# Performance work log

Measured on AMD Instinct MI355X. Metric: run time of the kernel, lower is better.

The kernel has to match this reference:

```python
import jax, jax.numpy as jnp
import numpy as np

N_NODES = 50000
N_EDGES = 150000
NODE_F, EDGE_F = 4, 11
HID, HID_OUT = 512, 1024
VS, AS_, N_ACT = 2048, 2048, 1000


def _graph_conv(x, W, b, src, dst, n, edge_weight=None):
    # DGL GraphConv, norm='both': D_out^{-1/2} on src feats, sum-aggregate, D_in^{-1/2} on dst.
    deg_out = jnp.maximum(jnp.zeros((n,), x.dtype).at[src].add(1.0), 1.0)
    deg_in = jnp.maximum(jnp.zeros((n,), x.dtype).at[dst].add(1.0), 1.0)
    h = x * (deg_out[:, None] ** -0.5)
    mult_first = W.shape[0] > W.shape[1]
    if mult_first:
        h = h @ W
    m = h[src]  # [E, d] gather
    if edge_weight is not None:
        m = m * edge_weight  # elementwise u_mul_e
    agg = jax.ops.segment_sum(m, dst, num_segments=n)
    if not mult_first:
        agg = agg @ W
    return agg * (deg_in[:, None] ** -0.5) + b


def setup_inputs() -> dict:
    key = jax.random.key(0)
    ks = jax.random.split(key, 16)
    s = 0.05
    return {
        'node_feats': jax.random.normal(ks[0], (N_NODES, NODE_F), jnp.float32),
        'edge_feats': jax.random.normal(ks[1], (N_EDGES, EDGE_F), jnp.float32),
        'W1': jax.random.normal(ks[2], (NODE_F, EDGE_F), jnp.float32) * s,
        'b1': jnp.zeros((EDGE_F,), jnp.float32),
        'W2': jax.random.normal(ks[3], (EDGE_F, HID), jnp.float32) * s,
        'b2': jnp.zeros((HID,), jnp.float32),
        'W3': jax.random.normal(ks[4], (HID, HID_OUT), jnp.float32) * s,
        'b3': jnp.zeros((HID_OUT,), jnp.float32),
        'Wv1': jax.random.normal(ks[5], (HID_OUT, VS), jnp.float32) * s,
        'bv1': jnp.zeros((VS,), jnp.float32),
        'Wv2': jax.random.normal(ks[6], (VS, 1), jnp.float32) * s,
        'bv2': jnp.zeros((1,), jnp.float32),
        'Wa1': jax.random.normal(ks[7], (HID_OUT, AS_), jnp.float32) * s,
        'ba1': jnp.zeros((AS_,), jnp.float32),
        'Wa2': jax.random.normal(ks[8], (AS_, N_ACT), jnp.float32) * s,
        'ba2': jnp.zeros((N_ACT,), jnp.float32),
        'src': jax.random.randint(ks[9], (N_EDGES,), 0, N_NODES, jnp.int32),
        'dst': jax.random.randint(ks[10], (N_EDGES,), 0, N_NODES, jnp.int32),
    }


def reference(node_feats, edge_feats, W1, b1, W2, b2, W3, b3,
              Wv1, bv1, Wv2, bv2, Wa1, ba1, Wa2, ba2, src, dst):
    n = node_feats.shape[0]
    loop = jnp.arange(n, dtype=src.dtype)
    srcL = jnp.concatenate([src, loop])  # add_self_loop
    dstL = jnp.concatenate([dst, loop])
    # self-loop edges get zero edge features (DGL default)
    ef = jnp.concatenate([edge_feats, jnp.zeros((n, edge_feats.shape[1]), edge_feats.dtype)], axis=0)

    h = jax.nn.relu(_graph_conv(node_feats, W1, b1, srcL, dstL, n))          # [N, 11]
    h = jax.nn.relu(_graph_conv(h, W2, b2, srcL, dstL, n, edge_weight=ef))   # [N, 512]
    h = _graph_conv(h, W3, b3, srcL, dstL, n)                                # [N, 1024]

    g_emb = jnp.mean(h, axis=0, keepdims=True)  # dgl.mean_nodes, single graph -> [1, 1024]

    v = jax.nn.relu(g_emb @ Wv1 + bv1) @ Wv2 + bv2        # [1, 1]
    a = jax.nn.relu(g_emb @ Wa1 + ba1) @ Wa2 + ba2        # [1, N_ACT]
    return v + (a - a.mean())
```

## Files before the change

kernel.cpp:

```cpp
#include <hip/hip_runtime.h>

#define NN 50000
#define NE 150000
#define NB 196

__global__ __launch_bounds__(256) void k_deg(const int* __restrict__ src,
                                             const int* __restrict__ dst,
                                             int* __restrict__ deg_out,
                                             int* __restrict__ deg_in) {
    int e = blockIdx.x * 256 + threadIdx.x;
    if (e < NE) {
        atomicAdd(&deg_out[src[e]], 1);
        atomicAdd(&deg_in[dst[e]], 1);
    }
}

__global__ __launch_bounds__(256) void k_bsum(const int* __restrict__ deg_in,
                                              const int* __restrict__ deg_out,
                                              int* __restrict__ bsum_in,
                                              int* __restrict__ bsum_out) {
    __shared__ int si[256], so[256];
    int t = threadIdx.x;
    int idx = blockIdx.x * 256 + t;
    si[t] = (idx < NN) ? deg_in[idx] : 0;
    so[t] = (idx < NN) ? deg_out[idx] : 0;
    __syncthreads();
    for (int off = 128; off >= 1; off >>= 1) {
        if (t < off) { si[t] += si[t + off]; so[t] += so[t + off]; }
        __syncthreads();
    }
    if (t == 0) { bsum_in[blockIdx.x] = si[0]; bsum_out[blockIdx.x] = so[0]; }
}

__global__ __launch_bounds__(256) void k_rowptr(const int* __restrict__ deg_in,
                                                const int* __restrict__ deg_out,
                                                const int* __restrict__ bsum_in,
                                                const int* __restrict__ bsum_out,
                                                int* __restrict__ rp_in,
                                                int* __restrict__ rp_out) {
    __shared__ int si[256], so[256];
    int b = blockIdx.x, t = threadIdx.x;
    si[t] = (t < b) ? bsum_in[t] : 0;
    so[t] = (t < b) ? bsum_out[t] : 0;
    __syncthreads();
    for (int off = 128; off >= 1; off >>= 1) {
        if (t < off) { si[t] += si[t + off]; so[t] += so[t + off]; }
        __syncthreads();
    }
    int off_in = si[0], off_out = so[0];
    __syncthreads();
    int idx = b * 256 + t;
    int di = (idx < NN) ? deg_in[idx] : 0;
    int dq = (idx < NN) ? deg_out[idx] : 0;
    si[t] = di; so[t] = dq;
    __syncthreads();
    for (int off = 1; off < 256; off <<= 1) {
        int a = (t >= off) ? si[t - off] : 0;
        int c2 = (t >= off) ? so[t - off] : 0;
        __syncthreads();
        si[t] += a; so[t] += c2;
        __syncthreads();
    }
    if (idx < NN) {
        rp_in[idx]  = off_in  + si[t] - di;
        rp_out[idx] = off_out + so[t] - dq;
    }
    if (b == 0 && t == 0) { rp_in[NN] = NE; rp_out[NN] = NE; }
}

__global__ __launch_bounds__(256) void k_scatter(const int* __restrict__ src,
                                                 const int* __restrict__ dst,
                                                 const int* __restrict__ rp_in,
                                                 const int* __restrict__ rp_out,
                                                 int* __restrict__ cur_in,
                                                 int* __restrict__ cur_out,
                                                 int* __restrict__ eidx_in,
                                                 int* __restrict__ nbr_out) {
    int e = blockIdx.x * 256 + threadIdx.x;
    if (e >= NE) return;
    int s = src[e], d = dst[e];
    int pi = rp_in[d] + atomicAdd(&cur_in[d], 1);
    eidx_in[pi] = e;
    int po = rp_out[s] + atomicAdd(&cur_out[s], 1);
    nbr_out[po] = d;
}

__global__ __launch_bounds__(256) void k_conv1g(const float* __restrict__ x,
                                                const int* __restrict__ src,
                                                const int* __restrict__ eidx_in,
                                                const int* __restrict__ rp_in,
                                                const int* __restrict__ nbr_out,
                                                const int* __restrict__ rp_out,
                                                const int* __restrict__ deg_out,
                                                const int* __restrict__ deg_in,
                                                const float* __restrict__ W1,
                                                const float* __restrict__ b1,
                                                float* __restrict__ h1s,
                                                float* __restrict__ c) {
    int n = blockIdx.x * 256 + threadIdx.x;
    if (n >= NN) return;
    float din  = rsqrtf((float)(deg_in[n] + 1));
    float dout = rsqrtf((float)(deg_out[n] + 1));
    const float4 xn = ((const float4*)x)[n];
    float a0 = xn.x * dout, a1 = xn.y * dout, a2 = xn.z * dout, a3 = xn.w * dout;
    int beg = rp_in[n], end = rp_in[n + 1];
    for (int p = beg; p < end; p++) {
        int e = eidx_in[p];
        int s = src[e];
        float ds = rsqrtf((float)(deg_out[s] + 1));
        float4 xs = ((const float4*)x)[s];
        a0 = fmaf(xs.x, ds, a0);
        a1 = fmaf(xs.y, ds, a1);
        a2 = fmaf(xs.z, ds, a2);
        a3 = fmaf(xs.w, ds, a3);
    }
    float cacc = din;
    int ob = rp_out[n], oe = rp_out[n + 1];
    for (int p = ob; p < oe; p++) {
        int d = nbr_out[p];
        cacc += rsqrtf((float)(deg_in[d] + 1));
    }
    c[n] = cacc;
    #pragma unroll
    for (int j = 0; j < 11; j++) {
        float y = a0 * W1[0 * 11 + j] + a1 * W1[1 * 11 + j] +
                  a2 * W1[2 * 11 + j] + a3 * W1[3 * 11 + j];
        y = fmaxf(fmaf(y, din, b1[j]), 0.f);
        h1s[n * 11 + j] = y * dout;
    }
}

__global__ __launch_bounds__(256) void k_agg2g(const float* __restrict__ h1s,
                                               const float* __restrict__ ef,
                                               const int* __restrict__ src,
                                               const int* __restrict__ eidx_in,
                                               const int* __restrict__ rp_in,
                                               float* __restrict__ agg2) {
    int tid = threadIdx.x;
    if (tid >= 253) return;
    int n = blockIdx.x * 23 + tid / 11;
    int j = tid % 11;
    if (n >= NN) return;
    int beg = rp_in[n], end = rp_in[n + 1];
    float acc = 0.f;
    for (int p = beg; p < end; p++) {
        int e = eidx_in[p];
        int s = src[e];
        acc = fmaf(h1s[s * 11 + j], ef[e * 11 + j], acc);
    }
    agg2[n * 11 + j] = acc;
}

#define NPB 64
__global__ __launch_bounds__(512) void k_conv2_reduce(const float* __restrict__ agg2,
                                                      const float* __restrict__ W2,
                                                      const float* __restrict__ b2,
                                                      const float* __restrict__ c,
                                                      const int* __restrict__ deg_out,
                                                      const int* __restrict__ deg_in,
                                                      float* __restrict__ t) {
    __shared__ float tile[NPB * 11];
    __shared__ float din_sh[NPB], w_sh[NPB];
    int n0 = blockIdx.x * NPB;
    int tid = threadIdx.x;
    for (int i = tid; i < NPB * 11; i += 512) {
        int gi = n0 * 11 + i;
        tile[i] = (gi < NN * 11) ? agg2[gi] : 0.f;
    }
    if (tid < NPB) {
        int node = n0 + tid;
        if (node < NN) {
            din_sh[tid] = rsqrtf((float)(deg_in[node] + 1));
            w_sh[tid]   = c[node] * rsqrtf((float)(deg_out[node] + 1)) * (1.0f / NN);
        } else { din_sh[tid] = 0.f; w_sh[tid] = 0.f; }
    }
    __syncthreads();
    float w[11];
    #pragma unroll
    for (int j = 0; j < 11; j++) w[j] = W2[j * 512 + tid];
    float bias = b2[tid];
    float acc = 0.f;
    for (int i = 0; i < NPB; i++) {
        float dot = 0.f;
        #pragma unroll
        for (int j = 0; j < 11; j++) dot = fmaf(tile[i * 11 + j], w[j], dot);
        float y = fmaxf(fmaf(dot, din_sh[i], bias), 0.f);
        acc = fmaf(w_sh[i], y, acc);
    }
    atomicAdd(&t[tid], acc);
}

__global__ __launch_bounds__(256) void k_g(const float* __restrict__ t,
                                           const float* __restrict__ W3,
                                           const float* __restrict__ b3,
                                           float* __restrict__ g) {
    int b = blockIdx.x;
    int oc = b & 3, kc = b >> 2;
    int o = oc * 256 + threadIdx.x;
    int k0 = kc * 32;
    __shared__ float ts[32];
    if (threadIdx.x < 32) ts[threadIdx.x] = t[k0 + threadIdx.x];
    __syncthreads();
    float acc = (kc == 0) ? b3[o] : 0.f;
    #pragma unroll 8
    for (int k = 0; k < 32; k++) acc = fmaf(ts[k], W3[(size_t)(k0 + k) * 1024 + o], acc);
    atomicAdd(&g[o], acc);
}

__global__ __launch_bounds__(256) void k_heads1(const float* __restrict__ g,
                                                const float* __restrict__ Wv1,
                                                const float* __restrict__ Wa1,
                                                float* __restrict__ hv_raw,
                                                float* __restrict__ ha_raw) {
    int b = blockIdx.x;
    int oc = b >> 4, kc = b & 15;
    int idx = oc * 256 + threadIdx.x;
    int k0 = kc * 64;
    __shared__ float gs[64];
    if (threadIdx.x < 64) gs[threadIdx.x] = g[k0 + threadIdx.x];
    __syncthreads();
    const float* W; float* outp; int o;
    if (idx < 2048) { W = Wv1; outp = hv_raw; o = idx; }
    else            { W = Wa1; outp = ha_raw; o = idx - 2048; }
    float acc = 0.f;
    #pragma unroll 8
    for (int k = 0; k < 64; k++) acc = fmaf(gs[k], W[(size_t)(k0 + k) * 2048 + o], acc);
    atomicAdd(&outp[o], acc);
}

__global__ __launch_bounds__(256) void k_heads2(const float* __restrict__ hv_raw,
                                                const float* __restrict__ bv1,
                                                const float* __restrict__ ha_raw,
                                                const float* __restrict__ ba1,
                                                const float* __restrict__ Wv2,
                                                const float* __restrict__ bv2,
                                                const float* __restrict__ Wa2,
                                                float* __restrict__ a_acc,
                                                float* __restrict__ v) {
    int b = blockIdx.x;
    int tid = threadIdx.x;
    if (b < 128) {
        int oc = b >> 5, kc = b & 31;
        int k0 = kc * 64;
        __shared__ float hs[64];
        if (tid < 64) hs[tid] = fmaxf(ha_raw[k0 + tid] + ba1[k0 + tid], 0.f);
        __syncthreads();
        int o = oc * 256 + tid;
        if (o < 1000) {
            float acc = 0.f;
            #pragma unroll 8
            for (int k = 0; k < 64; k++)
                acc = fmaf(hs[k], Wa2[(size_t)(k0 + k) * 1000 + o], acc);
            atomicAdd(&a_acc[o], acc);
        }
    } else {
        __shared__ float red[256];
        float acc = 0.f;
        for (int k = tid; k < 2048; k += 256)
            acc = fmaf(fmaxf(hv_raw[k] + bv1[k], 0.f), Wv2[k], acc);
        red[tid] = acc;
        __syncthreads();
        for (int s = 128; s >= 1; s >>= 1) {
            if (tid < s) red[tid] += red[tid + s];
            __syncthreads();
        }
        if (tid == 0) *v = red[0] + bv2[0];
    }
}

__global__ __launch_bounds__(1024) void k_final(const float* __restrict__ a_acc,
                                                const float* __restrict__ ba2,
                                                const float* __restrict__ vptr,
                                                float* __restrict__ out) {
    __shared__ float red[1024];
    int tid = threadIdx.x;
    float ai = (tid < 1000) ? a_acc[tid] + ba2[tid] : 0.f;
    red[tid] = ai;
    __syncthreads();
    for (int s = 512; s >= 1; s >>= 1) {
        if (tid < s) red[tid] += red[tid + s];
        __syncthreads();
    }
    float amean = red[0] * (1.0f / 1000.0f);
    if (tid < 1000) out[tid] = vptr[0] + ai - amean;
}

extern "C" void kernel_launch(void* const* d_in, const int* in_sizes, int n_in,
                              void* d_out, int out_size, void* d_ws, size_t ws_size,
                              hipStream_t stream) {
    const float* x   = (const float*)d_in[0];
    const float* ef  = (const float*)d_in[1];
    const float* W1  = (const float*)d_in[2];
    const float* b1  = (const float*)d_in[3];
    const float* W2  = (const float*)d_in[4];
    const float* b2  = (const float*)d_in[5];
    const float* W3  = (const float*)d_in[6];
    const float* b3  = (const float*)d_in[7];
    const float* Wv1 = (const float*)d_in[8];
    const float* bv1 = (const float*)d_in[9];
    const float* Wv2 = (const float*)d_in[10];
    const float* bv2 = (const float*)d_in[11];
    const float* Wa1 = (const float*)d_in[12];
    const float* ba1 = (const float*)d_in[13];
    const float* Wa2 = (const float*)d_in[14];
    const float* ba2 = (const float*)d_in[15];
    const int*   src = (const int*)d_in[16];
    const int*   dst = (const int*)d_in[17];
    float* out = (float*)d_out;

    char* ws = (char*)d_ws;
    size_t off = 0;
    auto alloc = [&](size_t bytes) -> void* {
        void* p = ws + off;
        off = (off + bytes + 255) & ~(size_t)255;
        return p;
    };
    int*   deg_out = (int*)  alloc(NN * 4);
    int*   deg_in  = (int*)  alloc(NN * 4);
    int*   cur_in  = (int*)  alloc(NN * 4);
    int*   cur_out = (int*)  alloc(NN * 4);
    float* t       = (float*)alloc(512 * 4);
    float* g       = (float*)alloc(1024 * 4);
    float* hv_raw  = (float*)alloc(2048 * 4);
    float* ha_raw  = (float*)alloc(2048 * 4);
    float* a_acc   = (float*)alloc(1024 * 4);
    size_t zero_bytes = off;
    int*   bsum_in  = (int*)  alloc(NB * 4);
    int*   bsum_out = (int*)  alloc(NB * 4);
    int*   rp_in    = (int*)  alloc((NN + 1) * 4);
    int*   rp_out   = (int*)  alloc((NN + 1) * 4);
    int*   eidx_in  = (int*)  alloc((size_t)NE * 4);
    int*   nbr_out  = (int*)  alloc((size_t)NE * 4);
    float* c        = (float*)alloc(NN * 4);
    float* h1s      = (float*)alloc((size_t)NN * 11 * 4);
    float* agg2     = (float*)alloc((size_t)NN * 11 * 4);
    float* v        = (float*)alloc(256);

    hipMemsetAsync(d_ws, 0, zero_bytes, stream);

    k_deg<<<(NE + 255) / 256, 256, 0, stream>>>(src, dst, deg_out, deg_in);
    k_bsum<<<NB, 256, 0, stream>>>(deg_in, deg_out, bsum_in, bsum_out);
    k_rowptr<<<NB, 256, 0, stream>>>(deg_in, deg_out, bsum_in, bsum_out, rp_in, rp_out);
    k_scatter<<<(NE + 255) / 256, 256, 0, stream>>>(src, dst, rp_in, rp_out,
                                                    cur_in, cur_out, eidx_in, nbr_out);
    k_conv1g<<<(NN + 255) / 256, 256, 0, stream>>>(x, src, eidx_in, rp_in, nbr_out, rp_out,
                                                   deg_out, deg_in, W1, b1, h1s, c);
    k_agg2g<<<(NN + 22) / 23, 256, 0, stream>>>(h1s, ef, src, eidx_in, rp_in, agg2);
    k_conv2_reduce<<<(NN + NPB - 1) / NPB, 512, 0, stream>>>(agg2, W2, b2, c, deg_out, deg_in, t);
    k_g<<<64, 256, 0, stream>>>(t, W3, b3, g);
    k_heads1<<<256, 256, 0, stream>>>(g, Wv1, Wa1, hv_raw, ha_raw);
    k_heads2<<<129, 256, 0, stream>>>(hv_raw, bv1, ha_raw, ba1, Wv2, bv2, Wa2, a_acc, v);
    k_final<<<1, 1024, 0, stream>>>(a_acc, ba2, v, out);
}
```

Before: 208.7 us.

## Replace CSR build and gathers with edge-parallel atomic scatter; fuse final reduction

```diff
diff --git a/kernel.cpp b/kernel.cpp
--- a/kernel.cpp
+++ b/kernel.cpp
@@ -2,7 +2,6 @@
 
 #define NN 50000
 #define NE 150000
-#define NB 196
 
 __global__ __launch_bounds__(256) void k_deg(const int* __restrict__ src,
                                              const int* __restrict__ dst,
@@ -15,112 +14,45 @@
     }
 }
 
-__global__ __launch_bounds__(256) void k_bsum(const int* __restrict__ deg_in,
-                                              const int* __restrict__ deg_out,
-                                              int* __restrict__ bsum_in,
-                                              int* __restrict__ bsum_out) {
-    __shared__ int si[256], so[256];
-    int t = threadIdx.x;
-    int idx = blockIdx.x * 256 + t;
-    si[t] = (idx < NN) ? deg_in[idx] : 0;
-    so[t] = (idx < NN) ? deg_out[idx] : 0;
-    __syncthreads();
-    for (int off = 128; off >= 1; off >>= 1) {
-        if (t < off) { si[t] += si[t + off]; so[t] += so[t + off]; }
-        __syncthreads();
-    }
-    if (t == 0) { bsum_in[blockIdx.x] = si[0]; bsum_out[blockIdx.x] = so[0]; }
-}
-
-__global__ __launch_bounds__(256) void k_rowptr(const int* __restrict__ deg_in,
-                                                const int* __restrict__ deg_out,
-                                                const int* __restrict__ bsum_in,
-                                                const int* __restrict__ bsum_out,
-                                                int* __restrict__ rp_in,
-                                                int* __restrict__ rp_out) {
-    __shared__ int si[256], so[256];
-    int b = blockIdx.x, t = threadIdx.x;
-    si[t] = (t < b) ? bsum_in[t] : 0;
-    so[t] = (t < b) ? bsum_out[t] : 0;
-    __syncthreads();
-    for (int off = 128; off >= 1; off >>= 1) {
-        if (t < off) { si[t] += si[t + off]; so[t] += so[t + off]; }
-        __syncthreads();
-    }
-    int off_in = si[0], off_out = so[0];
-    __syncthreads();
-    int idx = b * 256 + t;
-    int di = (idx < NN) ? deg_in[idx] : 0;
-    int dq = (idx < NN) ? deg_out[idx] : 0;
-    si[t] = di; so[t] = dq;
-    __syncthreads();
-    for (int off = 1; off < 256; off <<= 1) {
-        int a = (t >= off) ? si[t - off] : 0;
-        int c2 = (t >= off) ? so[t - off] : 0;
-        __syncthreads();
-        si[t] += a; so[t] += c2;
-        __syncthreads();
-    }
-    if (idx < NN) {
-        rp_in[idx]  = off_in  + si[t] - di;
-        rp_out[idx] = off_out + so[t] - dq;
-    }
-    if (b == 0 && t == 0) { rp_in[NN] = NE; rp_out[NN] = NE; }
-}
-
-__global__ __launch_bounds__(256) void k_scatter(const int* __restrict__ src,
-                                                 const int* __restrict__ dst,
-                                                 const int* __restrict__ rp_in,
-                                                 const int* __restrict__ rp_out,
-                                                 int* __restrict__ cur_in,
-                                                 int* __restrict__ cur_out,
-                                                 int* __restrict__ eidx_in,
-                                                 int* __restrict__ nbr_out) {
+__global__ __launch_bounds__(256) void k_edge1(const int* __restrict__ src,
+                                               const int* __restrict__ dst,
+                                               const int* __restrict__ deg_out,
+                                               const int* __restrict__ deg_in,
+                                               const float* __restrict__ x,
+                                               float* __restrict__ agg1,
+                                               float* __restrict__ c) {
     int e = blockIdx.x * 256 + threadIdx.x;
     if (e >= NE) return;
     int s = src[e], d = dst[e];
-    int pi = rp_in[d] + atomicAdd(&cur_in[d], 1);
-    eidx_in[pi] = e;
-    int po = rp_out[s] + atomicAdd(&cur_out[s], 1);
-    nbr_out[po] = d;
-}
-
-__global__ __launch_bounds__(256) void k_conv1g(const float* __restrict__ x,
-                                                const int* __restrict__ src,
-                                                const int* __restrict__ eidx_in,
-                                                const int* __restrict__ rp_in,
-                                                const int* __restrict__ nbr_out,
-                                                const int* __restrict__ rp_out,
-                                                const int* __restrict__ deg_out,
-                                                const int* __restrict__ deg_in,
-                                                const float* __restrict__ W1,
-                                                const float* __restrict__ b1,
-                                                float* __restrict__ h1s,
-                                                float* __restrict__ c) {
+    float ds = rsqrtf((float)(deg_out[s] + 1));
+    float dd = rsqrtf((float)(deg_in[d] + 1));
+    const float4 xs = ((const float4*)x)[s];
+    atomicAdd(&agg1[d * 4 + 0], xs.x * ds);
+    atomicAdd(&agg1[d * 4 + 1], xs.y * ds);
+    atomicAdd(&agg1[d * 4 + 2], xs.z * ds);
+    atomicAdd(&agg1[d * 4 + 3], xs.w * ds);
+    atomicAdd(&c[s], dd);
+}
+
+__global__ __launch_bounds__(256) void k_conv1(const float* __restrict__ x,
+                                               const int* __restrict__ deg_out,
+                                               const int* __restrict__ deg_in,
+                                               const float* __restrict__ agg1,
+                                               const float* __restrict__ W1,
+                                               const float* __restrict__ b1,
+                                               float* __restrict__ h1s,
+                                               float* __restrict__ c) {
     int n = blockIdx.x * 256 + threadIdx.x;
     if (n >= NN) return;
     float din  = rsqrtf((float)(deg_in[n] + 1));
     float dout = rsqrtf((float)(deg_out[n] + 1));
     const float4 xn = ((const float4*)x)[n];
-    float a0 = xn.x * dout, a1 = xn.y * dout, a2 = xn.z * dout, a3 = xn.w * dout;
-    int beg = rp_in[n], end = rp_in[n + 1];
-    for (int p = beg; p < end; p++) {
-        int e = eidx_in[p];
-        int s = src[e];
-        float ds = rsqrtf((float)(deg_out[s] + 1));
-        float4 xs = ((const float4*)x)[s];
-        a0 = fmaf(xs.x, ds, a0);
-        a1 = fmaf(xs.y, ds, a1);
-        a2 = fmaf(xs.z, ds, a2);
-        a3 = fmaf(xs.w, ds, a3);
-    }
-    float cacc = din;
-    int ob = rp_out[n], oe = rp_out[n + 1];
-    for (int p = ob; p < oe; p++) {
-        int d = nbr_out[p];
-        cacc += rsqrtf((float)(deg_in[d] + 1));
-    }
-    c[n] = cacc;
+    const float4 ag = ((const float4*)agg1)[n];
+    float a0 = ag.x + xn.x * dout;
+    float a1 = ag.y + xn.y * dout;
+    float a2 = ag.z + xn.z * dout;
+    float a3 = ag.w + xn.w * dout;
+    c[n] += din;
     #pragma unroll
     for (int j = 0; j < 11; j++) {
         float y = a0 * W1[0 * 11 + j] + a1 * W1[1 * 11 + j] +
@@ -130,25 +62,17 @@
     }
 }
 
-__global__ __launch_bounds__(256) void k_agg2g(const float* __restrict__ h1s,
+__global__ __launch_bounds__(256) void k_edge2(const int* __restrict__ src,
+                                               const int* __restrict__ dst,
+                                               const float* __restrict__ h1s,
                                                const float* __restrict__ ef,
-                                               const int* __restrict__ src,
-                                               const int* __restrict__ eidx_in,
-                                               const int* __restrict__ rp_in,
                                                float* __restrict__ agg2) {
-    int tid = threadIdx.x;
-    if (tid >= 253) return;
-    int n = blockIdx.x * 23 + tid / 11;
-    int j = tid % 11;
-    if (n >= NN) return;
-    int beg = rp_in[n], end = rp_in[n + 1];
-    float acc = 0.f;
-    for (int p = beg; p < end; p++) {
-        int e = eidx_in[p];
-        int s = src[e];
-        acc = fmaf(h1s[s * 11 + j], ef[e * 11 + j], acc);
-    }
-    agg2[n * 11 + j] = acc;
+    int T = blockIdx.x * 256 + threadIdx.x;
+    if (T >= NE * 11) return;
+    int e = T / 11;
+    int j = T - e * 11;
+    int s = src[e], d = dst[e];
+    atomicAdd(&agg2[d * 11 + j], h1s[s * 11 + j] * ef[T]);
 }
 
 #define NPB 64
@@ -228,61 +152,79 @@
     atomicAdd(&outp[o], acc);
 }
 
-__global__ __launch_bounds__(256) void k_heads2(const float* __restrict__ hv_raw,
-                                                const float* __restrict__ bv1,
-                                                const float* __restrict__ ha_raw,
-                                                const float* __restrict__ ba1,
-                                                const float* __restrict__ Wv2,
-                                                const float* __restrict__ bv2,
-                                                const float* __restrict__ Wa2,
-                                                float* __restrict__ a_acc,
-                                                float* __restrict__ v) {
+__global__ __launch_bounds__(256) void k_heads2f(const float* __restrict__ hv_raw,
+                                                 const float* __restrict__ bv1,
+                                                 const float* __restrict__ ha_raw,
+                                                 const float* __restrict__ ba1,
+                                                 const float* __restrict__ Wv2,
+                                                 const float* __restrict__ bv2,
+                                                 const float* __restrict__ Wa2,
+                                                 const float* __restrict__ ba2,
+                                                 float* __restrict__ a_acc,
+                                                 float* __restrict__ v,
+                                                 int* __restrict__ done,
+                                                 float* __restrict__ out) {
+    __shared__ float sh[256];
+    __shared__ int lastFlag;
     int b = blockIdx.x;
     int tid = threadIdx.x;
     if (b < 128) {
         int oc = b >> 5, kc = b & 31;
         int k0 = kc * 64;
-        __shared__ float hs[64];
-        if (tid < 64) hs[tid] = fmaxf(ha_raw[k0 + tid] + ba1[k0 + tid], 0.f);
+        if (tid < 64) sh[tid] = fmaxf(ha_raw[k0 + tid] + ba1[k0 + tid], 0.f);
         __syncthreads();
         int o = oc * 256 + tid;
         if (o < 1000) {
             float acc = 0.f;
             #pragma unroll 8
             for (int k = 0; k < 64; k++)
-                acc = fmaf(hs[k], Wa2[(size_t)(k0 + k) * 1000 + o], acc);
+                acc = fmaf(sh[k], Wa2[(size_t)(k0 + k) * 1000 + o], acc);
             atomicAdd(&a_acc[o], acc);
         }
     } else {
-        __shared__ float red[256];
         float acc = 0.f;
         for (int k = tid; k < 2048; k += 256)
             acc = fmaf(fmaxf(hv_raw[k] + bv1[k], 0.f), Wv2[k], acc);
-        red[tid] = acc;
+        sh[tid] = acc;
         __syncthreads();
         for (int s = 128; s >= 1; s >>= 1) {
-            if (tid < s) red[tid] += red[tid + s];
+            if (tid < s) sh[tid] += sh[tid + s];
             __syncthreads();
         }
-        if (tid == 0) *v = red[0] + bv2[0];
-    }
-}
-
-__global__ __launch_bounds__(1024) void k_final(const float* __restrict__ a_acc,
-                                                const float* __restrict__ ba2,
-                                                const float* __restrict__ vptr,
-                                                float* __restrict__ out) {
-    __shared__ float red[1024];
-    int tid = threadIdx.x;
-    float ai = (tid < 1000) ? a_acc[tid] + ba2[tid] : 0.f;
-    red[tid] = ai;
-    __syncthreads();
-    for (int s = 512; s >= 1; s >>= 1) {
-        if (tid < s) red[tid] += red[tid + s];
+        if (tid == 0) *v = sh[0] + bv2[0];
+    }
+    __syncthreads();
+    if (tid == 0) {
+        __threadfence();
+        int old = atomicAdd(done, 1);
+        lastFlag = (old == 128) ? 1 : 0;
+    }
+    __syncthreads();
+    if (!lastFlag) return;
+    __threadfence();
+    float ai[4];
+    float lsum = 0.f;
+    #pragma unroll
+    for (int k = 0; k < 4; k++) {
+        int idx = tid + k * 256;
+        float val = (idx < 1000) ? a_acc[idx] + ba2[idx] : 0.f;
+        ai[k] = val;
+        lsum += val;
+    }
+    __syncthreads();
+    sh[tid] = lsum;
+    __syncthreads();
+    for (int s = 128; s >= 1; s >>= 1) {
+        if (tid < s) sh[tid] += sh[tid + s];
         __syncthreads();
     }
-    float amean = red[0] * (1.0f / 1000.0f);
-    if (tid < 1000) out[tid] = vptr[0] + ai - amean;
+    float amean = sh[0] * (1.0f / 1000.0f);
+    float vv = *v;
+    #pragma unroll
+    for (int k = 0; k < 4; k++) {
+        int idx = tid + k * 256;
+        if (idx < 1000) out[idx] = vv + ai[k] - amean;
+    }
 }
 
 extern "C" void kernel_launch(void* const* d_in, const int* in_sizes, int n_in,
@@ -317,38 +259,28 @@
     };
     int*   deg_out = (int*)  alloc(NN * 4);
     int*   deg_in  = (int*)  alloc(NN * 4);
-    int*   cur_in  = (int*)  alloc(NN * 4);
-    int*   cur_out = (int*)  alloc(NN * 4);
+    float* agg1    = (float*)alloc((size_t)NN * 4 * 4);
+    float* c       = (float*)alloc(NN * 4);
+    float* agg2    = (float*)alloc((size_t)NN * 11 * 4);
     float* t       = (float*)alloc(512 * 4);
     float* g       = (float*)alloc(1024 * 4);
     float* hv_raw  = (float*)alloc(2048 * 4);
     float* ha_raw  = (float*)alloc(2048 * 4);
     float* a_acc   = (float*)alloc(1024 * 4);
+    int*   done    = (int*)  alloc(256);
     size_t zero_bytes = off;
-    int*   bsum_in  = (int*)  alloc(NB * 4);
-    int*   bsum_out = (int*)  alloc(NB * 4);
-    int*   rp_in    = (int*)  alloc((NN + 1) * 4);
-    int*   rp_out   = (int*)  alloc((NN + 1) * 4);
-    int*   eidx_in  = (int*)  alloc((size_t)NE * 4);
-    int*   nbr_out  = (int*)  alloc((size_t)NE * 4);
-    float* c        = (float*)alloc(NN * 4);
-    float* h1s      = (float*)alloc((size_t)NN * 11 * 4);
-    float* agg2     = (float*)alloc((size_t)NN * 11 * 4);
-    float* v        = (float*)alloc(256);
+    float* h1s     = (float*)alloc((size_t)NN * 11 * 4);
+    float* v       = (float*)alloc(256);
 
     hipMemsetAsync(d_ws, 0, zero_bytes, stream);
 
     k_deg<<<(NE + 255) / 256, 256, 0, stream>>>(src, dst, deg_out, deg_in);
-    k_bsum<<<NB, 256, 0, stream>>>(deg_in, deg_out, bsum_in, bsum_out);
-    k_rowptr<<<NB, 256, 0, stream>>>(deg_in, deg_out, bsum_in, bsum_out, rp_in, rp_out);
-    k_scatter<<<(NE + 255) / 256, 256, 0, stream>>>(src, dst, rp_in, rp_out,
-                                                    cur_in, cur_out, eidx_in, nbr_out);
-    k_conv1g<<<(NN + 255) / 256, 256, 0, stream>>>(x, src, eidx_in, rp_in, nbr_out, rp_out,
-                                                   deg_out, deg_in, W1, b1, h1s, c);
-    k_agg2g<<<(NN + 22) / 23, 256, 0, stream>>>(h1s, ef, src, eidx_in, rp_in, agg2);
+    k_edge1<<<(NE + 255) / 256, 256, 0, stream>>>(src, dst, deg_out, deg_in, x, agg1, c);
+    k_conv1<<<(NN + 255) / 256, 256, 0, stream>>>(x, deg_out, deg_in, agg1, W1, b1, h1s, c);
+    k_edge2<<<(NE * 11 + 255) / 256, 256, 0, stream>>>(src, dst, h1s, ef, agg2);
     k_conv2_reduce<<<(NN + NPB - 1) / NPB, 512, 0, stream>>>(agg2, W2, b2, c, deg_out, deg_in, t);
     k_g<<<64, 256, 0, stream>>>(t, W3, b3, g);
     k_heads1<<<256, 256, 0, stream>>>(g, Wv1, Wa1, hv_raw, ha_raw);
-    k_heads2<<<129, 256, 0, stream>>>(hv_raw, bv1, ha_raw, ba1, Wv2, bv2, Wa2, a_acc, v);
-    k_final<<<1, 1024, 0, stream>>>(a_acc, ba2, v, out);
-}
+    k_heads2f<<<129, 256, 0, stream>>>(hv_raw, bv1, ha_raw, ba1, Wv2, bv2, Wa2, ba2,
+                                       a_acc, v, done, out);
+}
```

New measurement: 228.5 us. 1.1x slower.
